# Optimization experiments

Hardware: AMD Instinct MI355X
Metric: run time of the kernel (lower is better)

The kernel has to match this reference:

```python
import jax, jax.numpy as jnp
import numpy as np


def setup_inputs() -> dict:
    key = jax.random.key(0)
    k = jax.random.split(key, 6)
    B, N, Cin, Cd, nE = 64, 197, 768, 256, 8192
    return {
        "z": jax.random.normal(k[0], (B, N, Cin), dtype=jnp.float32),
        "emb": jax.random.truncated_normal(k[1], -3.0, 3.0, (nE, Cd), dtype=jnp.float32),
        "W_compress": jax.random.normal(k[2], (Cin, Cd), dtype=jnp.float32) * 0.02,
        "b_compress": jnp.zeros((Cd,), dtype=jnp.float32),
        "W_expand": jax.random.normal(k[3], (Cd, Cin), dtype=jnp.float32) * 0.02,
        "b_expand": jnp.zeros((Cin,), dtype=jnp.float32),
    }


def reference(z, emb, W_compress, b_compress, W_expand, b_expand):
    # compress: [B,N,Cin] -> [B,N,Cd]
    zc = jnp.einsum('bnc,cd->bnd', z, W_compress) + b_compress
    zf = zc.reshape(-1, zc.shape[-1])  # [M, Cd]
    # squared distances to codebook: ||z||^2 + ||e||^2 - 2 z.e  -> [M, nE]
    d = (jnp.sum(zf * zf, axis=1, keepdims=True)
         + jnp.sum(emb * emb, axis=1)
         - 2.0 * (zf @ emb.T))
    indices = jnp.argmin(d, axis=1)  # [M]
    z_q = emb[indices]               # gather [M, Cd]
    sg = jax.lax.stop_gradient
    # training-mode commitment/codebook loss
    loss = jnp.mean((sg(z_q) - zf) ** 2) + 2.0 * jnp.mean((z_q - sg(zf)) ** 2)
    # straight-through estimator
    z_q = sg(z_q) + zf - sg(zf)
    z_q = z_q.reshape(zc.shape)
    out = jnp.einsum('bnd,dc->bnc', z_q, W_expand) + b_expand  # [B,N,Cin]
    return (out, loss)
```

## Files before the change

kernel.cpp:

```cpp
#include <hip/hip_runtime.h>
#include <stdint.h>

#define M_TOK 12608
#define MPAD  12672
#define CIN   768
#define CD    256
#define NE    8192
#define NCHUNK 8
#define CHUNK  1024

typedef unsigned long long u64;
typedef unsigned int u32;
typedef _Float16 f16;
typedef _Float16 f16x8 __attribute__((ext_vector_type(8)));
typedef _Float16 f16x4 __attribute__((ext_vector_type(4)));
typedef float f32x4 __attribute__((ext_vector_type(4)));

#if __has_builtin(__builtin_amdgcn_global_load_lds)
#define HAVE_GLL 1
#else
#define HAVE_GLL 0
#endif

__device__ __forceinline__ void stage16(const f16* src, char* lds_base, int lane)
{
#if HAVE_GLL
    __builtin_amdgcn_global_load_lds(
        (__attribute__((address_space(1))) void*)(src),
        (__attribute__((address_space(3))) void*)(lds_base), 16, 0, 0);
#else
    *(f16x8*)(lds_base + lane * 16) = *(const f16x8*)src;
#endif
}

__global__ __launch_bounds__(256) void k_prep(const float* __restrict__ emb,
                                              const float* __restrict__ Wc,
                                              const float* __restrict__ We,
                                              const float* __restrict__ z,
                                              float* __restrict__ enorm,
                                              f16* __restrict__ embf16,
                                              f16* __restrict__ wchi,
                                              f16* __restrict__ wclo,
                                              f16* __restrict__ wet,
                                              f16* __restrict__ zhi,
                                              f16* __restrict__ zlo,
                                              float* __restrict__ loss_slot)
{
    const int b = blockIdx.x;
    const int t = threadIdx.x;
    if (b < 2048) {
        if (b == 0 && t == 0) *loss_slot = 0.0f;
        int row  = b * 4 + (t >> 6);
        int lane = t & 63;
        float4 v = *(const float4*)&emb[(size_t)row * CD + lane * 4];
        f16x4 hv = { (f16)v.x, (f16)v.y, (f16)v.z, (f16)v.w };
        *(f16x4*)&embf16[(size_t)row * CD + lane * 4] = hv;
        float s = v.x*v.x + v.y*v.y + v.z*v.z + v.w*v.w;
        #pragma unroll
        for (int o = 32; o; o >>= 1) s += __shfl_down(s, o, 64);
        if (lane == 0) enorm[row] = s;
    } else if (b < 2048 + 768) {
        int tid = (b - 2048) * 256 + t;
        {
            int n = tid & 255, k = tid >> 8;
            float v = Wc[(size_t)k * CD + n];
            f16 h = (f16)v;
            wchi[(size_t)n * CIN + k] = h;
            wclo[(size_t)n * CIN + k] = (f16)(v - (float)h);
        }
        {
            int d = tid / CIN, c = tid - d * CIN;
            wet[(size_t)c * CD + d] = (f16)We[(size_t)d * CIN + c];
        }
    } else {
        size_t i4 = (size_t)(b - 2816) * 256 + t;
        float4 v = ((const float4*)z)[i4];
        f16x4 h = { (f16)v.x, (f16)v.y, (f16)v.z, (f16)v.w };
        f16x4 lo = { (f16)(v.x - (float)h.x), (f16)(v.y - (float)h.y),
                     (f16)(v.z - (float)h.z), (f16)(v.w - (float)h.w) };
        ((f16x4*)zhi)[i4] = h;
        ((f16x4*)zlo)[i4] = lo;
    }
}

__global__ __launch_bounds__(256) void k_compress_f(const f16* __restrict__ zhi,
                                                    const f16* __restrict__ zlo,
                                                    const f16* __restrict__ wchi,
                                                    const f16* __restrict__ wclo,
                                                    const float* __restrict__ bc,
                                                    float* __restrict__ zc,
                                                    f16* __restrict__ zcf16)
{
    __shared__ __align__(16) f16 Ah[128 * 64];
    __shared__ __align__(16) f16 Al[128 * 64];
    __shared__ __align__(16) f16 Bh[64 * 64];
    __shared__ __align__(16) f16 Bl[64 * 64];

    const int t = threadIdx.x;
    const int w = t >> 6, l = t & 63;
    const int wrow = w * 32;
    const int m0   = blockIdx.x * 128;
    const int col0 = blockIdx.y * 64;

    const int cg   = (t & 7) ^ ((t >> 3) & 7);
    const int rloc = t >> 3;
    const f16* ahsrc[4]; const f16* alsrc[4];
    #pragma unroll
    for (int i = 0; i < 4; ++i) {
        int am = m0 + i * 32 + rloc; am = am < M_TOK ? am : (M_TOK - 1);
        ahsrc[i] = zhi + (size_t)am * CIN + cg * 8;
        alsrc[i] = zlo + (size_t)am * CIN + cg * 8;
    }
    const f16* bhsrc[2]; const f16* blsrc[2];
    #pragma unroll
    for (int i = 0; i < 2; ++i) {
        int br = col0 + i * 32 + rloc;
        bhsrc[i] = wchi + (size_t)br * CIN + cg * 8;
        blsrc[i] = wclo + (size_t)br * CIN + cg * 8;
    }

    f32x4 acc[2][4];
    #pragma unroll
    for (int a = 0; a < 2; ++a)
        #pragma unroll
        for (int b2 = 0; b2 < 4; ++b2) acc[a][b2] = (f32x4){0.f,0.f,0.f,0.f};

    for (int ks = 0; ks < CIN / 64; ++ks) {
        __syncthreads();
        #pragma unroll
        for (int i = 0; i < 4; ++i) {
            stage16(ahsrc[i] + ks * 64, (char*)Ah + (i * 256 + w * 64) * 16, l);
            stage16(alsrc[i] + ks * 64, (char*)Al + (i * 256 + w * 64) * 16, l);
        }
        #pragma unroll
        for (int i = 0; i < 2; ++i) {
            stage16(bhsrc[i] + ks * 64, (char*)Bh + (i * 256 + w * 64) * 16, l);
            stage16(blsrc[i] + ks * 64, (char*)Bl + (i * 256 + w * 64) * 16, l);
        }
        __syncthreads();
        #pragma unroll
        for (int kk = 0; kk < 2; ++kk) {
            const int pofs = ((kk * 4 + (l >> 4)) ^ (l & 7)) * 16;
            f16x8 ah[2], al[2], bh[4], bl[4];
            #pragma unroll
            for (int tm = 0; tm < 2; ++tm) {
                ah[tm] = *(const f16x8*)((const char*)Ah + (wrow + tm*16 + (l & 15)) * 128 + pofs);
                al[tm] = *(const f16x8*)((const char*)Al + (wrow + tm*16 + (l & 15)) * 128 + pofs);
            }
            #pragma unroll
            for (int tn = 0; tn < 4; ++tn) {
                bh[tn] = *(const f16x8*)((const char*)Bh + (tn*16 + (l & 15)) * 128 + pofs);
                bl[tn] = *(const f16x8*)((const char*)Bl + (tn*16 + (l & 15)) * 128 + pofs);
            }
            #pragma unroll
            for (int tm = 0; tm < 2; ++tm)
                #pragma unroll
                for (int tn = 0; tn < 4; ++tn) {
                    f32x4 a = acc[tm][tn];
                    a = __builtin_amdgcn_mfma_f32_16x16x32_f16(ah[tm], bh[tn], a, 0, 0, 0);
                    a = __builtin_amdgcn_mfma_f32_16x16x32_f16(ah[tm], bl[tn], a, 0, 0, 0);
                    a = __builtin_amdgcn_mfma_f32_16x16x32_f16(al[tm], bh[tn], a, 0, 0, 0);
                    acc[tm][tn] = a;
                }
        }
    }

    #pragma unroll
    for (int tm = 0; tm < 2; ++tm) {
        #pragma unroll
        for (int reg = 0; reg < 4; ++reg) {
            int row = m0 + wrow + tm * 16 + (l >> 4) * 4 + reg;
            if (row < M_TOK) {
                #pragma unroll
                for (int tn = 0; tn < 4; ++tn) {
                    int col = col0 + tn * 16 + (l & 15);
                    float v = acc[tm][tn][reg] + bc[col];
                    zc[(size_t)row * CD + col] = v;
                    zcf16[(size_t)row * CD + col] = (f16)v;
                }
            }
        }
    }
}

__global__ __launch_bounds__(256, 2) void k_dist_mfma(const f16* __restrict__ zcf16,
                                                      const f16* __restrict__ embf16,
                                                      const float* __restrict__ enorm,
                                                      u64* __restrict__ part)
{
    __shared__ __align__(16) f16 As[128 * 64];
    __shared__ __align__(16) f16 Bs[256 * 64];
    __shared__ u64 wred[128][2][2];

    const int t = threadIdx.x;
    const int w = t >> 6, l = t & 63;
    const int wrow  = (w >> 1) * 64;
    const int wcolh = (w & 1);
    const int m0    = blockIdx.x * 128;
    const int chunk = blockIdx.y;

    const int cg   = (t & 7) ^ ((t >> 3) & 7);
    const int rloc = t >> 3;
    const f16* asrc[4];
    #pragma unroll
    for (int i = 0; i < 4; ++i) {
        int am = m0 + i * 32 + rloc; am = am < M_TOK ? am : (M_TOK - 1);
        asrc[i] = zcf16 + (size_t)am * CD + cg * 8;
    }

    float bd[16];
    int   bcol[16];
    #pragma unroll
    for (int s = 0; s < 16; ++s) { bd[s] = __builtin_inff(); bcol[s] = 0; }

    for (int jp = 0; jp < 4; ++jp) {
        const int j0 = chunk * CHUNK + jp * 256;
        const f16* bbase = embf16 + (size_t)(j0 + rloc) * CD + cg * 8;

        f32x4 acc[4][8];
        #pragma unroll
        for (int a = 0; a < 4; ++a)
            #pragma unroll
            for (int b2 = 0; b2 < 8; ++b2) acc[a][b2] = (f32x4){0.f,0.f,0.f,0.f};

        for (int ks = 0; ks < 4; ++ks) {
            __syncthreads();
            #pragma unroll
            for (int i = 0; i < 4; ++i)
                stage16(asrc[i] + ks * 64, (char*)As + (i * 256 + w * 64) * 16, l);
            #pragma unroll
            for (int i = 0; i < 8; ++i)
                stage16(bbase + (size_t)i * 32 * CD + ks * 64,
                        (char*)Bs + (i * 256 + w * 64) * 16, l);
            __syncthreads();
            #pragma unroll
            for (int kk = 0; kk < 2; ++kk) {
                const int pofs = ((kk * 4 + (l >> 4)) ^ (l & 7)) * 16;
                f16x8 af[4], bf[8];
                #pragma unroll
                for (int tm = 0; tm < 4; ++tm)
                    af[tm] = *(const f16x8*)((const char*)As + (wrow + tm*16 + (l & 15)) * 128 + pofs);
                #pragma unroll
                for (int tn = 0; tn < 8; ++tn)
                    bf[tn] = *(const f16x8*)((const char*)Bs + (wcolh*128 + tn*16 + (l & 15)) * 128 + pofs);
                #pragma unroll
                for (int tm = 0; tm < 4; ++tm)
                    #pragma unroll
                    for (int tn = 0; tn < 8; ++tn)
                        acc[tm][tn] = __builtin_amdgcn_mfma_f32_16x16x32_f16(af[tm], bf[tn], acc[tm][tn], 0, 0, 0);
            }
        }

        const int cb = j0 + wcolh * 128 + (l & 15);
        float en[8];
        #pragma unroll
        for (int tn = 0; tn < 8; ++tn) en[tn] = enorm[cb + tn * 16];
        #pragma unroll
        for (int tm = 0; tm < 4; ++tm) {
            #pragma unroll
            for (int reg = 0; reg < 4; ++reg) {
                const int s = tm * 4 + reg;
                float dm = bd[s]; int cm = bcol[s];
                #pragma unroll
                for (int tn = 0; tn < 8; ++tn) {
                    float d = fmaf(acc[tm][tn][reg], -2.f, en[tn]);
                    bool lt = d < dm;
                    dm = lt ? d : dm;
                    cm = lt ? cb + tn * 16 : cm;
                }
                bd[s] = dm; bcol[s] = cm;
            }
        }
    }

    #pragma unroll
    for (int tm = 0; tm < 4; ++tm) {
        #pragma unroll
        for (int reg = 0; reg < 4; ++reg) {
            const int s = tm * 4 + reg;
            u32 u = __float_as_uint(bd[s]);
            u = (u & 0x80000000u) ? ~u : (u | 0x80000000u);
            u64 b  = ((u64)u << 32) | (u32)bcol[s];
            u64 sc = ~0ull;
            #pragma unroll
            for (int off = 1; off <= 8; off <<= 1) {
                u64 ob = __shfl_xor(b, off, 64);
                u64 os = __shfl_xor(sc, off, 64);
                u64 nb = b < ob ? b : ob;
                u64 mx = b < ob ? ob : b;
                sc = sc < os ? sc : os;
                sc = sc < mx ? sc : mx;
                b = nb;
            }
            if ((l & 15) == 0) {
                int row = wrow + tm * 16 + (l >> 4) * 4 + reg;
                wred[row][w & 1][0] = b;
                wred[row][w & 1][1] = sc;
            }
        }
    }
    __syncthreads();
    if (t < 128) {
        u64 b0 = wred[t][0][0], s0 = wred[t][0][1];
        u64 b1 = wred[t][1][0], s1 = wred[t][1][1];
        u64 B  = b0 < b1 ? b0 : b1;
        u64 mx = b0 < b1 ? b1 : b0;
        u64 S  = s0 < s1 ? s0 : s1;
        S = S < mx ? S : mx;
        int row = m0 + t;
        if (row < M_TOK) {
            part[((size_t)row * NCHUNK + chunk) * 2 + 0] = B;
            part[((size_t)row * NCHUNK + chunk) * 2 + 1] = S;
        }
    }
}

__global__ __launch_bounds__(256) void k_rescore(const float* __restrict__ zc,
                                                 const float* __restrict__ emb,
                                                 const float* __restrict__ enorm,
                                                 const u64* __restrict__ part,
                                                 int* __restrict__ idxp,
                                                 float* __restrict__ loss_slot)
{
    const int row = blockIdx.x * 4 + (threadIdx.x >> 6);
    const int l   = threadIdx.x & 63;
    __shared__ float lsum[4];

    float4 zr = *(const float4*)&zc[(size_t)row * CD + l * 4];
    u64 best = ~0ull;
    for (int c = 0; c < 16; ++c) {
        u64 key = part[(size_t)row * 16 + c];
        int col = (int)((u32)key & (NE - 1));
        float4 er = *(const float4*)&emb[(size_t)col * CD + l * 4];
        float p = zr.x*er.x + zr.y*er.y + zr.z*er.z + zr.w*er.w;
        #pragma unroll
        for (int o = 32; o; o >>= 1) p += __shfl_xor(p, o, 64);
        float d = fmaf(p, -2.f, enorm[col]);
        u32 u = __float_as_uint(d);
        u = (u & 0x80000000u) ? ~u : (u | 0x80000000u);
        u64 k2 = ((u64)u << 32) | (u32)col;
        best = k2 < best ? k2 : best;
    }
    float zn = zr.x*zr.x + zr.y*zr.y + zr.z*zr.z + zr.w*zr.w;
    #pragma unroll
    for (int o = 32; o; o >>= 1) zn += __shfl_xor(zn, o, 64);

    u32 hi = (u32)(best >> 32);
    float dbest = (hi & 0x80000000u) ? __uint_as_float(hi & 0x7fffffffu)
                                     : __uint_as_float(~hi);
    if (l == 0) {
        idxp[row] = (int)((u32)best & (NE - 1));
        lsum[threadIdx.x >> 6] = dbest + zn;
    }
    __syncthreads();
    if (threadIdx.x == 0) {
        float tot = lsum[0] + lsum[1] + lsum[2] + lsum[3];
        atomicAdd(loss_slot, tot * (3.0f / 3227648.0f));
    }
}

__global__ __launch_bounds__(256) void k_expand_mfma(const f16* __restrict__ embf16,
                                                     const int* __restrict__ idxp,
                                                     const f16* __restrict__ wet,
                                                     const float* __restrict__ be,
                                                     float* __restrict__ out)
{
    __shared__ __align__(16) f16 As[128 * 64];
    __shared__ __align__(16) f16 Bs[128 * 64];

    const int t = threadIdx.x;
    const int w = t >> 6, l = t & 63;
    const int wrow = (w >> 1) * 64, wcol = (w & 1) * 64;
    const int m0   = blockIdx.x * 128;
    const int col0 = blockIdx.y * 128;

    const int cg   = (t & 7) ^ ((t >> 3) & 7);
    const int rloc = t >> 3;
    const f16* asrc[4]; const f16* bsrc[4];
    #pragma unroll
    for (int i = 0; i < 4; ++i) {
        int r = i * 32 + rloc;
        int m = m0 + r; m = m < M_TOK ? m : (M_TOK - 1);
        int er = idxp[m];
        asrc[i] = embf16 + (size_t)er * CD + cg * 8;
        bsrc[i] = wet + (size_t)(col0 + r) * CD + cg * 8;
    }
    const int prd0 = (l >> 4) ^ (l & 7);
    const int prd1 = (4 + (l >> 4)) ^ (l & 7);

    f32x4 acc[4][4];
    #pragma unroll
    for (int a = 0; a < 4; ++a)
        #pragma unroll
        for (int b = 0; b < 4; ++b) acc[a][b] = (f32x4){0.f,0.f,0.f,0.f};

    for (int ks = 0; ks < 4; ++ks) {
        __syncthreads();
        #pragma unroll
        for (int i = 0; i < 4; ++i) {
            stage16(asrc[i] + ks * 64, (char*)As + (i * 256 + w * 64) * 16, l);
            stage16(bsrc[i] + ks * 64, (char*)Bs + (i * 256 + w * 64) * 16, l);
        }
        __syncthreads();
        #pragma unroll
        for (int kk = 0; kk < 2; ++kk) {
            const int pofs = (kk ? prd1 : prd0) * 16;
            f16x8 af[4], bf[4];
            #pragma unroll
            for (int tm = 0; tm < 4; ++tm)
                af[tm] = *(const f16x8*)((const char*)As + (wrow + tm*16 + (l & 15)) * 128 + pofs);
            #pragma unroll
            for (int tn = 0; tn < 4; ++tn)
                bf[tn] = *(const f16x8*)((const char*)Bs + (wcol + tn*16 + (l & 15)) * 128 + pofs);
            #pragma unroll
            for (int tm = 0; tm < 4; ++tm)
                #pragma unroll
                for (int tn = 0; tn < 4; ++tn)
                    acc[tm][tn] = __builtin_amdgcn_mfma_f32_16x16x32_f16(af[tm], bf[tn], acc[tm][tn], 0, 0, 0);
        }
    }

    float bev[4];
    #pragma unroll
    for (int tn = 0; tn < 4; ++tn) bev[tn] = be[col0 + wcol + tn * 16 + (l & 15)];
    #pragma unroll
    for (int tm = 0; tm < 4; ++tm) {
        #pragma unroll
        for (int reg = 0; reg < 4; ++reg) {
            int row = m0 + wrow + tm * 16 + (l >> 4) * 4 + reg;
            if (row < M_TOK) {
                #pragma unroll
                for (int tn = 0; tn < 4; ++tn) {
                    int col = col0 + wcol + tn * 16 + (l & 15);
                    out[(size_t)row * CIN + col] = acc[tm][tn][reg] + bev[tn];
                }
            }
        }
    }
}

#define BK1 16
__global__ __launch_bounds__(256) void k_compress(const float* __restrict__ z,
                                                  const float* __restrict__ W,
                                                  const float* __restrict__ bias,
                                                  float* __restrict__ zc,
                                                  f16* __restrict__ zcf16)
{
    __shared__ __align__(16) float As[BK1][64 + 4];
    __shared__ __align__(16) float Bs[BK1][64 + 4];
    const int t  = threadIdx.x;
    const int tx = t & 15, ty = t >> 4;
    const int row0 = blockIdx.x * 64;
    const int col0 = blockIdx.y * 64;

    const int la_r = t >> 2;
    const int la_k = (t & 3) << 2;
    const int lb_k = t >> 4;
    const int lb_n = (t & 15) << 2;

    float acc[4][4] = {};

    for (int k0 = 0; k0 < CIN; k0 += BK1) {
        float4 a4 = *(const float4*)&z[(size_t)(row0 + la_r) * CIN + k0 + la_k];
        float4 b4 = *(const float4*)&W[(size_t)(k0 + lb_k) * CD + col0 + lb_n];
        __syncthreads();
        As[la_k + 0][la_r] = a4.x; As[la_k + 1][la_r] = a4.y;
        As[la_k + 2][la_r] = a4.z; As[la_k + 3][la_r] = a4.w;
        *(float4*)&Bs[lb_k][lb_n] = b4;
        __syncthreads();
        #pragma unroll
        for (int k = 0; k < BK1; ++k) {
            float a[4], b[4];
            *(float4*)&a[0] = *(const float4*)&As[k][ty * 4];
            *(float4*)&b[0] = *(const float4*)&Bs[k][tx * 4];
            #pragma unroll
            for (int i = 0; i < 4; ++i)
                #pragma unroll
                for (int j = 0; j < 4; ++j)
                    acc[i][j] = fmaf(a[i], b[j], acc[i][j]);
        }
    }

    float4 bb = *(const float4*)&bias[col0 + tx * 4];
    #pragma unroll
    for (int i = 0; i < 4; ++i) {
        float4 v;
        v.x = acc[i][0] + bb.x; v.y = acc[i][1] + bb.y;
        v.z = acc[i][2] + bb.z; v.w = acc[i][3] + bb.w;
        size_t off = (size_t)(row0 + ty * 4 + i) * CD + col0 + tx * 4;
        *(float4*)&zc[off] = v;
        f16x4 hv = { (f16)v.x, (f16)v.y, (f16)v.z, (f16)v.w };
        *(f16x4*)&zcf16[off] = hv;
    }
}

extern "C" void kernel_launch(void* const* d_in, const int* in_sizes, int n_in,
                              void* d_out, int out_size, void* d_ws, size_t ws_size,
                              hipStream_t stream)
{
    (void)in_sizes; (void)n_in; (void)out_size;

    const float* z   = (const float*)d_in[0];
    const float* emb = (const float*)d_in[1];
    const float* Wc  = (const float*)d_in[2];
    const float* bc  = (const float*)d_in[3];
    const float* We  = (const float*)d_in[4];
    const float* be  = (const float*)d_in[5];

    float* out       = (float*)d_out;
    float* loss_slot = out + (size_t)M_TOK * CIN;

    char* base = (char*)d_ws;
    size_t off = 0;
    auto align_up = [](size_t x) { return (x + 255) & ~(size_t)255; };

    float* enorm = (float*)(base + off); off = align_up(off + (size_t)NE * 4);
    u64*   part  = (u64*)(base + off);   off = align_up(off + (size_t)M_TOK * 16 * 8);
    int*   idxp  = (int*)(base + off);   off = align_up(off + (size_t)M_TOK * 4);
    f16*   embf16= (f16*)(base + off);   off = align_up(off + (size_t)NE * CD * 2);
    f16*   zcf16 = (f16*)(base + off);   off = align_up(off + (size_t)MPAD * CD * 2);
    f16*   wet   = (f16*)(base + off);   off = align_up(off + (size_t)CIN * CD * 2);
    f16*   wchi  = (f16*)(base + off);   off = align_up(off + (size_t)CD * CIN * 2);
    f16*   wclo  = (f16*)(base + off);   off = align_up(off + (size_t)CD * CIN * 2);

    const size_t zsplit_bytes = (size_t)M_TOK * CIN * 2;
    bool have_split = (ws_size >= off + 2 * zsplit_bytes);
    f16 *zhi = nullptr, *zlo = nullptr;
    if (have_split) {
        zhi = (f16*)(base + off); off = align_up(off + zsplit_bytes);
        zlo = (f16*)(base + off); off = align_up(off + zsplit_bytes);
    }
    const size_t zc_bytes = (size_t)M_TOK * CD * 4;
    float* zc = (ws_size >= off + zc_bytes) ? (float*)(base + off) : out;

    if (have_split) {
        k_prep      <<<12272, 256, 0, stream>>>(emb, Wc, We, z, enorm, embf16,
                                                wchi, wclo, wet, zhi, zlo, loss_slot);
        k_compress_f<<<dim3(MPAD / 128, CD / 64), 256, 0, stream>>>(zhi, zlo, wchi, wclo,
                                                                    bc, zc, zcf16);
    } else {
        k_prep    <<<2816, 256, 0, stream>>>(emb, Wc, We, z, enorm, embf16,
                                             wchi, wclo, wet, (f16*)wchi, (f16*)wclo, loss_slot);
        k_compress<<<dim3(M_TOK / 64, CD / 64), 256, 0, stream>>>(z, Wc, bc, zc, zcf16);
    }

    k_dist_mfma  <<<dim3(MPAD / 128, NCHUNK), 256, 0, stream>>>(zcf16, embf16, enorm, part);
    k_rescore    <<<M_TOK / 4, 256, 0, stream>>>(zc, emb, enorm, part, idxp, loss_slot);
    k_expand_mfma<<<dim3(MPAD / 128, CIN / 128), 256, 0, stream>>>(embf16, idxp, wet, be, out);
}
```

Before: 324.2 us.

## Keep query tile in registers and pack tile index into distance low bits

The distance kernel now loads each warp's 64x256 fp16 query rows into registers once, instead of staging them through LDS for every codebook tile. It streams the codebook in 64-row tiles into a swizzled LDS buffer. The running argmin now stores the tile index in the low 4 mantissa bits of the distance, so tracking the best column needs only a float min instead of a compare plus select. The aim is to cut LDS traffic, barriers and per-element argmin work. In exchange it raises register pressure (32 f16x8 fragments per thread) and perturbs distances slightly. That perturbation can change which entry wins on near-ties, although the later refine step using the second-best value may absorb this.

After: 285.2 us. 12.0% less time.

```diff
diff --git a/kernel.cpp b/kernel.cpp
--- a/kernel.cpp
+++ b/kernel.cpp
@@ -188,114 +188,105 @@
                                                       const float* __restrict__ enorm,
                                                       u64* __restrict__ part)
 {
-    __shared__ __align__(16) f16 As[128 * 64];
-    __shared__ __align__(16) f16 Bs[256 * 64];
+    __shared__ __align__(16) f16 Bs[64 * 256];
     __shared__ u64 wred[128][2][2];
 
     const int t = threadIdx.x;
     const int w = t >> 6, l = t & 63;
-    const int wrow  = (w >> 1) * 64;
-    const int wcolh = (w & 1);
+    const int rg  = w >> 1;
+    const int cgp = w & 1;
     const int m0    = blockIdx.x * 128;
     const int chunk = blockIdx.y;
-
-    const int cg   = (t & 7) ^ ((t >> 3) & 7);
-    const int rloc = t >> 3;
-    const f16* asrc[4];
-    #pragma unroll
-    for (int i = 0; i < 4; ++i) {
-        int am = m0 + i * 32 + rloc; am = am < M_TOK ? am : (M_TOK - 1);
-        asrc[i] = zcf16 + (size_t)am * CD + cg * 8;
-    }
-
-    float bd[16];
-    int   bcol[16];
-    #pragma unroll
-    for (int s = 0; s < 16; ++s) { bd[s] = __builtin_inff(); bcol[s] = 0; }
-
-    for (int jp = 0; jp < 4; ++jp) {
-        const int j0 = chunk * CHUNK + jp * 256;
-        const f16* bbase = embf16 + (size_t)(j0 + rloc) * CD + cg * 8;
-
-        f32x4 acc[4][8];
-        #pragma unroll
-        for (int a = 0; a < 4; ++a)
-            #pragma unroll
-            for (int b2 = 0; b2 < 8; ++b2) acc[a][b2] = (f32x4){0.f,0.f,0.f,0.f};
-
-        for (int ks = 0; ks < 4; ++ks) {
-            __syncthreads();
-            #pragma unroll
-            for (int i = 0; i < 4; ++i)
-                stage16(asrc[i] + ks * 64, (char*)As + (i * 256 + w * 64) * 16, l);
-            #pragma unroll
-            for (int i = 0; i < 8; ++i)
-                stage16(bbase + (size_t)i * 32 * CD + ks * 64,
-                        (char*)Bs + (i * 256 + w * 64) * 16, l);
-            __syncthreads();
-            #pragma unroll
-            for (int kk = 0; kk < 2; ++kk) {
-                const int pofs = ((kk * 4 + (l >> 4)) ^ (l & 7)) * 16;
-                f16x8 af[4], bf[8];
-                #pragma unroll
-                for (int tm = 0; tm < 4; ++tm)
-                    af[tm] = *(const f16x8*)((const char*)As + (wrow + tm*16 + (l & 15)) * 128 + pofs);
-                #pragma unroll
-                for (int tn = 0; tn < 8; ++tn)
-                    bf[tn] = *(const f16x8*)((const char*)Bs + (wcolh*128 + tn*16 + (l & 15)) * 128 + pofs);
-                #pragma unroll
-                for (int tm = 0; tm < 4; ++tm)
-                    #pragma unroll
-                    for (int tn = 0; tn < 8; ++tn)
-                        acc[tm][tn] = __builtin_amdgcn_mfma_f32_16x16x32_f16(af[tm], bf[tn], acc[tm][tn], 0, 0, 0);
-            }
-        }
-
-        const int cb = j0 + wcolh * 128 + (l & 15);
-        float en[8];
-        #pragma unroll
-        for (int tn = 0; tn < 8; ++tn) en[tn] = enorm[cb + tn * 16];
-        #pragma unroll
-        for (int tm = 0; tm < 4; ++tm) {
-            #pragma unroll
-            for (int reg = 0; reg < 4; ++reg) {
-                const int s = tm * 4 + reg;
-                float dm = bd[s]; int cm = bcol[s];
-                #pragma unroll
-                for (int tn = 0; tn < 8; ++tn) {
-                    float d = fmaf(acc[tm][tn][reg], -2.f, en[tn]);
-                    bool lt = d < dm;
-                    dm = lt ? d : dm;
-                    cm = lt ? cb + tn * 16 : cm;
+    const int jbase = chunk * CHUNK;
+
+    f16x8 afr[4][8];
+    {
+        const int rbase = m0 + rg * 64 + (l & 15);
+        #pragma unroll
+        for (int mb = 0; mb < 4; ++mb) {
+            int r = rbase + mb * 16; r = r < M_TOK ? r : (M_TOK - 1);
+            const f16* p = zcf16 + (size_t)r * CD + (l >> 4) * 8;
+            #pragma unroll
+            for (int ks = 0; ks < 8; ++ks)
+                afr[mb][ks] = *(const f16x8*)(p + ks * 32);
+        }
+    }
+
+    float bd[2][16];
+    #pragma unroll
+    for (int sc = 0; sc < 2; ++sc)
+        #pragma unroll
+        for (int s = 0; s < 16; ++s) bd[sc][s] = __builtin_inff();
+
+    for (int jt = 0; jt < 16; ++jt) {
+        const int j0 = jbase + jt * 64;
+        __syncthreads();
+        #pragma unroll
+        for (int i = 0; i < 8; ++i) {
+            int r = (w * 8 + i) * 2 + (l >> 5);
+            int c = (l & 31) ^ (r & 7);
+            stage16(embf16 + (size_t)(j0 + r) * CD + c * 8,
+                    (char*)Bs + (w * 8 + i) * 1024, l);
+        }
+        __syncthreads();
+
+        #pragma unroll
+        for (int sc = 0; sc < 2; ++sc) {
+            const int colrow = cgp * 32 + sc * 16 + (l & 15);
+            f32x4 acc[4];
+            #pragma unroll
+            for (int mb = 0; mb < 4; ++mb) acc[mb] = (f32x4){0.f,0.f,0.f,0.f};
+            #pragma unroll
+            for (int ks = 0; ks < 8; ++ks) {
+                int pc = (ks * 4 + (l >> 4)) ^ (colrow & 7);
+                f16x8 bf = *(const f16x8*)((const char*)Bs + colrow * 512 + pc * 16);
+                #pragma unroll
+                for (int mb = 0; mb < 4; ++mb)
+                    acc[mb] = __builtin_amdgcn_mfma_f32_16x16x32_f16(afr[mb][ks], bf, acc[mb], 0, 0, 0);
+            }
+            float en = enorm[j0 + colrow];
+            #pragma unroll
+            for (int mb = 0; mb < 4; ++mb) {
+                #pragma unroll
+                for (int reg = 0; reg < 4; ++reg) {
+                    float d = fmaf(acc[mb][reg], -2.f, en);
+                    float ds = __uint_as_float((__float_as_uint(d) & ~15u) | (u32)jt);
+                    float cur = bd[sc][mb * 4 + reg];
+                    bd[sc][mb * 4 + reg] = ds < cur ? ds : cur;
                 }
-                bd[s] = dm; bcol[s] = cm;
-            }
-        }
-    }
-
-    #pragma unroll
-    for (int tm = 0; tm < 4; ++tm) {
+            }
+        }
+    }
+
+    #pragma unroll
+    for (int mb = 0; mb < 4; ++mb) {
         #pragma unroll
         for (int reg = 0; reg < 4; ++reg) {
-            const int s = tm * 4 + reg;
-            u32 u = __float_as_uint(bd[s]);
-            u = (u & 0x80000000u) ? ~u : (u | 0x80000000u);
-            u64 b  = ((u64)u << 32) | (u32)bcol[s];
-            u64 sc = ~0ull;
+            u64 key[2];
+            #pragma unroll
+            for (int sc = 0; sc < 2; ++sc) {
+                u32 bits = __float_as_uint(bd[sc][mb * 4 + reg]);
+                int jtb  = (int)(bits & 15u);
+                int col  = jbase + jtb * 64 + cgp * 32 + sc * 16 + (l & 15);
+                u32 u = (bits & 0x80000000u) ? ~bits : (bits | 0x80000000u);
+                key[sc] = ((u64)u << 32) | (u32)col;
+            }
+            u64 b  = key[0] < key[1] ? key[0] : key[1];
+            u64 s2 = key[0] < key[1] ? key[1] : key[0];
             #pragma unroll
             for (int off = 1; off <= 8; off <<= 1) {
                 u64 ob = __shfl_xor(b, off, 64);
-                u64 os = __shfl_xor(sc, off, 64);
+                u64 os = __shfl_xor(s2, off, 64);
                 u64 nb = b < ob ? b : ob;
                 u64 mx = b < ob ? ob : b;
-                sc = sc < os ? sc : os;
-                sc = sc < mx ? sc : mx;
+                s2 = s2 < os ? s2 : os;
+                s2 = s2 < mx ? s2 : mx;
                 b = nb;
             }
             if ((l & 15) == 0) {
-                int row = wrow + tm * 16 + (l >> 4) * 4 + reg;
-                wred[row][w & 1][0] = b;
-                wred[row][w & 1][1] = sc;
+                int row = rg * 64 + mb * 16 + (l >> 4) * 4 + reg;
+                wred[row][cgp][0] = b;
+                wred[row][cgp][1] = s2;
             }
         }
     }
```
